# Kernel tuning notes

Measured on AMD Instinct MI355X. Metric: run time of the kernel, lower is better.

## Reference

```python
import jax, jax.numpy as jnp
import numpy as np

KERNEL_SIZE = 13
SIGMA_MIN, SIGMA_MAX = 0.4, 10.0
BETA, THRESHOLD = 0.95, 1.0


@jax.custom_vjp
def spike(x):
    # Heaviside forward, snntorch ATan surrogate backward (alpha=2)
    return (x > 0).astype(x.dtype)

def _spike_fwd(x):
    return spike(x), x

def _spike_bwd(x, g):
    return (g / (1.0 + (jnp.pi * x) ** 2),)

spike.defvjp(_spike_fwd, _spike_bwd)


def setup_inputs() -> dict:
    key = jax.random.key(0)
    k1, k2 = jax.random.split(key)
    B, C, T = 32, 224, 2048
    inp = jax.random.normal(k1, (B, 1, C, T), dtype=jnp.float32)
    linear_w = jax.random.normal(k2, (1, C), dtype=jnp.float32) * (1.0 / np.sqrt(C))
    return {"inp": inp, "linear_w": linear_w}


def _forward(inp, linear_w):
    x = inp[:, 0]  # [B, C, T]
    B, C, T = x.shape
    sigma_mean = 0.5 * (SIGMA_MIN + SIGMA_MAX)
    # adaptive sigma per (batch, time): Linear over channel axis, no bias
    w = sigma_mean + jnp.einsum('bct,c->bt', x, linear_w[0]) * (SIGMA_MAX - SIGMA_MIN)
    w = jnp.clip(w, SIGMA_MIN, SIGMA_MAX)  # [B, T]

    half = KERNEL_SIZE // 2
    r = jnp.linspace(-half, half, KERNEL_SIZE)
    r_all = jnp.linspace(-half * 10, half * 10, KERNEL_SIZE * 10)
    sig = w[..., None]  # [B, T, 1]
    kern = jnp.exp(-0.5 * (r / sig) ** 2)                       # [B, T, K]
    norm = jnp.exp(-0.5 * (r_all / sig) ** 2).sum(-1, keepdims=True)
    kern = kern / norm                                          # normalized over fine grid

    # adaptive gaussian smoothing along the CHANNEL axis (per timestep kernel)
    xt = jnp.transpose(x, (0, 2, 1))                            # [B, T, C]
    padded = jnp.pad(xt, ((0, 0), (0, 0), (half, half)))        # zero pad channels
    x_mean = sum(padded[:, :, k:k + C] * kern[:, :, k:k + 1]
                 for k in range(KERNEL_SIZE))                   # [B, T, C]
    x_mean = jnp.transpose(x_mean, (0, 2, 1))                   # [B, C, T]

    I = x - jax.nn.relu(x - x_mean)                             # soft min(x, x_mean)

    # Leaky-integrate-and-fire over time (snntorch Leaky, reset-by-subtract)
    def step(mem, I_t):
        reset = jax.lax.stop_gradient((mem > THRESHOLD).astype(I_t.dtype))
        mem = BETA * mem + I_t - reset * THRESHOLD
        spk = spike(mem - THRESHOLD)
        return mem, spk

    I_seq = jnp.transpose(I, (2, 0, 1))                         # [T, B, C]
    _, spk = jax.lax.scan(step, jnp.zeros((B, C), I.dtype), I_seq)
    spk = jnp.transpose(spk, (1, 2, 0))                         # [B, C, T]
    return spk[:, None]                                         # [B, 1, C, T]


def reference(inp, linear_w):
    return _forward(inp, linear_w)
```

## Files before the change

kernel.cpp:

```cpp
#include <hip/hip_runtime.h>
#include <math.h>

#define BB 32
#define CCH 224
#define TTT 2048
#define TPB 128
#define NT  (TTT/TPB)
#define CG  28
#define NCG (CCH/CG)
#define IROW 29
#define CPW 4
#define NSLOT 7

__device__ __forceinline__ void bar_lds() {
    asm volatile("s_waitcnt lgkmcnt(0)" ::: "memory");
    __builtin_amdgcn_s_barrier();
    asm volatile("" ::: "memory");
}

__global__ __launch_bounds__(1024) void kw(
    const float* __restrict__ x, const float* __restrict__ lw,
    double* __restrict__ kernG)
{
    __shared__ double sp[4][256];
    const int b  = blockIdx.y;
    const int tl = threadIdx.x & 255;
    const int q  = threadIdx.x >> 8;
    const int t  = blockIdx.x * 256 + tl;

    const float* xb  = x + (((size_t)(b * CCH + 56 * q)) << 11) + t;
    const float* lwq = lw + 56 * q;

    double p = 0.0;
    #pragma unroll 8
    for (int i = 0; i < 56; ++i)
        p += (double)xb[(size_t)i << 11] * (double)lwq[i];
    sp[q][tl] = p;
    __syncthreads();

    if (threadIdx.x < 256) {
        const int tt = blockIdx.x * 256 + threadIdx.x;
        double acc = (sp[0][threadIdx.x] + sp[1][threadIdx.x])
                   + (sp[2][threadIdx.x] + sp[3][threadIdx.x]);

        double w = 5.2 + acc * 9.6;
        w = fmin(fmax(w, 0.4), 10.0);
        double iw2 = 1.0 / (w * w);

        const double s = 120.0 / 129.0;
        double G  = exp(-0.125 * s * s * iw2);
        double G2 = G * G, G4 = G2 * G2, G8 = G4 * G4;
        double term = G, cmul = G8, norm = G;
        for (int u = 1; u <= 64; ++u) { term *= cmul; cmul *= G8; norm += term; }
        norm *= 2.0;

        double P = exp(-0.5 * iw2), P2 = P * P;
        double a = 1.0, bm = P, inv = 1.0 / norm;
        double* kr = kernG + (size_t)(b * TTT + tt) * 7;
        kr[0] = inv;
        #pragma unroll
        for (int d = 1; d <= 6; ++d) {
            a *= bm; bm *= P2;
            kr[d] = a * inv;
        }
    }
}

__global__ __launch_bounds__(512) void kf(
    const float* __restrict__ x, const double* __restrict__ kernG,
    float* __restrict__ out)
{
    __shared__ float IsR[NSLOT][TPB][IROW];
    __shared__ unsigned long long bitsb[2][2][CG][2];

    const int b   = blockIdx.y;
    const int cgi = blockIdx.x;
    const int c0  = cgi * CG;
    const int tid = threadIdx.x;
    const int ctid = tid - 64;

    const float*  xbase = x + (((size_t)(b * CCH)) << 11);
    const double* kbase = kernG + (size_t)(b * TTT) * 7;
    float* obase = out + (((size_t)(b * CCH + c0)) << 11);

    double mem = 0.0;
    bool   r   = false;

    const int tl = ctid & 63;
    const int cw = ctid >> 6;
    const int cb = CPW * cw;

    auto issue = [&](int tile, float (&rv)[2][16], double (&kv)[2][7]) {
        const int gt0 = tile * TPB;
        #pragma unroll
        for (int h = 0; h < 2; ++h) {
            const int tt = gt0 + tl + 64 * h;
            #pragma unroll
            for (int i = 0; i < 16; ++i) {
                int cr = c0 + cb - 6 + i;
                rv[h][i] = (cr >= 0 && cr < CCH)
                         ? xbase[((size_t)cr << 11) + tt] : 0.f;
            }
            const double* kp = kbase + (size_t)tt * 7;
            #pragma unroll
            for (int i = 0; i < 7; ++i) kv[h][i] = kp[i];
        }
    };

    auto conv_store = [&](int slot, float (&rv)[2][16], double (&kv)[2][7]) {
        #pragma unroll
        for (int h = 0; h < 2; ++h) {
            double kk7[7];
            #pragma unroll
            for (int i = 0; i < 7; ++i) kk7[i] = kv[h][i];
            double xv[16];
            #pragma unroll
            for (int i = 0; i < 16; ++i) xv[i] = (double)rv[h][i];
            #pragma unroll
            for (int c = 0; c < CPW; ++c) {
                double acc = 0.0;
                #pragma unroll
                for (int kk = 0; kk < 13; ++kk) {
                    int d = kk < 6 ? 6 - kk : kk - 6;
                    acc = fma(xv[c + kk], kk7[d], acc);
                }
                double xvv = xv[c + 6];
                double dd  = xvv - acc;
                IsR[slot][tl + 64 * h][cb + c] =
                    (float)(xvv - (dd > 0.0 ? dd : 0.0));
            }
        }
    };

    auto writeTile = [&](int t, int par, int seg) {
        const int t0o = t * TPB;
        const int c = ctid >> 4, q = ctid & 15;
        #pragma unroll
        for (int h = 0; h < 2; ++h) {
            unsigned long long bits = bitsb[par][seg][c][h] >> (4 * q);
            float4 v;
            v.x = (bits & 1ull) ? 1.0f : 0.0f;
            v.y = (bits & 2ull) ? 1.0f : 0.0f;
            v.z = (bits & 4ull) ? 1.0f : 0.0f;
            v.w = (bits & 8ull) ? 1.0f : 0.0f;
            *(float4*)(obase + ((size_t)c << 11) + t0o + 64 * h + 4 * q) = v;
        }
    };

    auto phase = [&](int k, float (&rv)[2][16], double (&kv)[2][7]) {
        if (tid >= 64) {
            if (k >= 2 && k <= 11) writeTile(k - 2, (k - 1) & 1, 0);
            if (k >= 7)            writeTile(k + 3, (k - 1) & 1, 1);
            if (k <= 10) conv_store((k + 5) % NSLOT, rv, kv);
            if (k <= 8)  issue(k + 7, rv, kv);
        } else {
            const int seg = tid >> 5;
            const int c   = tid & 31;
            const int myt = seg ? (k + 4) : (k - 1);
            const bool act = (c < CG) && (seg ? (k <= 11) : (k <= 10));
            __builtin_amdgcn_s_setprio(1);
            if (act) {
                const float* isb = &IsR[myt % NSLOT][0][c];
                unsigned long long bits0 = 0ull, bits1 = 0ull;
                double va[8], vb8[8], ca[8], cb2[8];
                #pragma unroll
                for (int j2 = 0; j2 < 8; ++j2) va[j2] = (double)isb[j2 * IROW];
                #pragma unroll
                for (int j2 = 0; j2 < 8; ++j2) ca[j2] = va[j2] - 1.0;
                for (int g2 = 0; g2 < TPB; g2 += 16) {
                    #pragma unroll
                    for (int j2 = 0; j2 < 8; ++j2)
                        vb8[j2] = (double)isb[(g2 + 8 + j2) * IROW];
                    #pragma unroll
                    for (int j2 = 0; j2 < 8; ++j2) cb2[j2] = vb8[j2] - 1.0;
                    #pragma unroll
                    for (int j2 = 0; j2 < 8; ++j2) {
                        double m1 = fma(0.95, mem, va[j2]);
                        double m2 = fma(0.95, mem, ca[j2]);
                        mem = r ? m2 : m1;
                        r = mem > 1.0;
                        const int s = g2 + j2;
                        unsigned long long bbit =
                            (unsigned long long)(r ? 1 : 0) << (s & 63);
                        if (s < 64) bits0 |= bbit; else bits1 |= bbit;
                    }
                    if (g2 + 16 < TPB) {
                        #pragma unroll
                        for (int j2 = 0; j2 < 8; ++j2)
                            va[j2] = (double)isb[(g2 + 16 + j2) * IROW];
                        #pragma unroll
                        for (int j2 = 0; j2 < 8; ++j2) ca[j2] = va[j2] - 1.0;
                    }
                    #pragma unroll
                    for (int j2 = 0; j2 < 8; ++j2) {
                        double m1 = fma(0.95, mem, vb8[j2]);
                        double m2 = fma(0.95, mem, cb2[j2]);
                        mem = r ? m2 : m1;
                        r = mem > 1.0;
                        const int s = g2 + 8 + j2;
                        unsigned long long bbit =
                            (unsigned long long)(r ? 1 : 0) << (s & 63);
                        if (s < 64) bits0 |= bbit; else bits1 |= bbit;
                    }
                }
                bitsb[k & 1][seg][c][0] = bits0;
                bitsb[k & 1][seg][c][1] = bits1;
            }
            __builtin_amdgcn_s_setprio(0);
        }
        bar_lds();
    };

    float  rA[2][16], rB[2][16];
    double kA[2][7],  kB[2][7];

    if (tid >= 64) {
        for (int i = 0; i < 6; ++i) {
            issue(i, rA, kA);
            conv_store(i, rA, kA);
        }
        issue(6, rB, kB);
        issue(7, rA, kA);
    }
    bar_lds();

    for (int kk = 1; kk <= 12; kk += 2) {
        phase(kk,     rB, kB);
        phase(kk + 1, rA, kA);
    }
}

extern "C" void kernel_launch(void* const* d_in, const int* in_sizes, int n_in,
                              void* d_out, int out_size, void* d_ws, size_t ws_size,
                              hipStream_t stream)
{
    const float* x  = (const float*)d_in[0];
    const float* lw = (const float*)d_in[1];
    float* out = (float*)d_out;

    double* kernG = (double*)d_ws;

    kw<<<dim3(TTT / 256, BB), 1024, 0, stream>>>(x, lw, kernG);
    kf<<<dim3(NCG, BB), 512, 0, stream>>>(x, kernG, out);
}
```

Before: 171.7 us.

## Transpose LDS current buffer, deepen slot ring, and restructure prologue pipeline

The staged current buffer is now laid out channel-major with padded rows, so the scan threads read consecutive timesteps with float2 LDS loads instead of strided scalar loads. The ring grows to eight slots using power-of-two indexing. The prologue software-pipelines global loads against convolution, and the main loop runs one fewer phase because the second scan segment starts one tile later. This aims to shorten the serial scan's LDS latency and the prologue stall, at the cost of more LDS and a retuned schedule that could be wrong.

```diff
diff --git a/kernel.cpp b/kernel.cpp
--- a/kernel.cpp
+++ b/kernel.cpp
@@ -8,9 +8,9 @@
 #define NT  (TTT/TPB)
 #define CG  28
 #define NCG (CCH/CG)
-#define IROW 29
 #define CPW 4
-#define NSLOT 7
+#define NSLOT 8
+#define TROW 130
 
 __device__ __forceinline__ void bar_lds() {
     asm volatile("s_waitcnt lgkmcnt(0)" ::: "memory");
@@ -70,7 +70,7 @@
     const float* __restrict__ x, const double* __restrict__ kernG,
     float* __restrict__ out)
 {
-    __shared__ float IsR[NSLOT][TPB][IROW];
+    __shared__ float IsT[NSLOT][CG][TROW];
     __shared__ unsigned long long bitsb[2][2][CG][2];
 
     const int b   = blockIdx.y;
@@ -126,7 +126,7 @@
                 }
                 double xvv = xv[c + 6];
                 double dd  = xvv - acc;
-                IsR[slot][tl + 64 * h][cb + c] =
+                IsT[slot][cb + c][tl + 64 * h] =
                     (float)(xvv - (dd > 0.0 ? dd : 0.0));
             }
         }
@@ -149,28 +149,34 @@
 
     auto phase = [&](int k, float (&rv)[2][16], double (&kv)[2][7]) {
         if (tid >= 64) {
-            if (k >= 2 && k <= 11) writeTile(k - 2, (k - 1) & 1, 0);
-            if (k >= 7)            writeTile(k + 3, (k - 1) & 1, 1);
-            if (k <= 10) conv_store((k + 5) % NSLOT, rv, kv);
-            if (k <= 8)  issue(k + 7, rv, kv);
-        } else {
+            if (k >= 2)  writeTile(k - 2, (k - 1) & 1, 0);
+            if (k >= 6)  writeTile(k + 4, (k - 1) & 1, 1);
+            if (k <= 9)  conv_store((k + 6) & 7, rv, kv);
+            if (k <= 7)  issue(k + 8, rv, kv);
+        } else if (k <= 10) {
             const int seg = tid >> 5;
             const int c   = tid & 31;
-            const int myt = seg ? (k + 4) : (k - 1);
-            const bool act = (c < CG) && (seg ? (k <= 11) : (k <= 10));
+            const int myt = seg ? (k + 5) : (k - 1);
             __builtin_amdgcn_s_setprio(1);
-            if (act) {
-                const float* isb = &IsR[myt % NSLOT][0][c];
+            if (c < CG) {
+                const float* isb = &IsT[myt & 7][c][0];
                 unsigned long long bits0 = 0ull, bits1 = 0ull;
                 double va[8], vb8[8], ca[8], cb2[8];
                 #pragma unroll
-                for (int j2 = 0; j2 < 8; ++j2) va[j2] = (double)isb[j2 * IROW];
+                for (int j2 = 0; j2 < 4; ++j2) {
+                    float2 p2 = *(const float2*)(isb + 2 * j2);
+                    va[2 * j2]     = (double)p2.x;
+                    va[2 * j2 + 1] = (double)p2.y;
+                }
                 #pragma unroll
                 for (int j2 = 0; j2 < 8; ++j2) ca[j2] = va[j2] - 1.0;
                 for (int g2 = 0; g2 < TPB; g2 += 16) {
                     #pragma unroll
-                    for (int j2 = 0; j2 < 8; ++j2)
-                        vb8[j2] = (double)isb[(g2 + 8 + j2) * IROW];
+                    for (int j2 = 0; j2 < 4; ++j2) {
+                        float2 p2 = *(const float2*)(isb + g2 + 8 + 2 * j2);
+                        vb8[2 * j2]     = (double)p2.x;
+                        vb8[2 * j2 + 1] = (double)p2.y;
+                    }
                     #pragma unroll
                     for (int j2 = 0; j2 < 8; ++j2) cb2[j2] = vb8[j2] - 1.0;
                     #pragma unroll
@@ -186,8 +192,11 @@
                     }
                     if (g2 + 16 < TPB) {
                         #pragma unroll
-                        for (int j2 = 0; j2 < 8; ++j2)
-                            va[j2] = (double)isb[(g2 + 16 + j2) * IROW];
+                        for (int j2 = 0; j2 < 4; ++j2) {
+                            float2 p2 = *(const float2*)(isb + g2 + 16 + 2 * j2);
+                            va[2 * j2]     = (double)p2.x;
+                            va[2 * j2 + 1] = (double)p2.y;
+                        }
                         #pragma unroll
                         for (int j2 = 0; j2 < 8; ++j2) ca[j2] = va[j2] - 1.0;
                     }
@@ -215,18 +224,20 @@
     double kA[2][7],  kB[2][7];
 
     if (tid >= 64) {
-        for (int i = 0; i < 6; ++i) {
-            issue(i, rA, kA);
-            conv_store(i, rA, kA);
-        }
-        issue(6, rB, kB);
-        issue(7, rA, kA);
+        issue(0, rA, kA); issue(1, rB, kB);
+        conv_store(0, rA, kA); issue(2, rA, kA);
+        conv_store(1, rB, kB); issue(3, rB, kB);
+        conv_store(2, rA, kA); issue(4, rA, kA);
+        conv_store(3, rB, kB); issue(5, rB, kB);
+        conv_store(4, rA, kA); issue(6, rA, kA);
+        conv_store(5, rB, kB); issue(7, rB, kB);
+        conv_store(6, rA, kA); issue(8, rA, kA);
     }
     bar_lds();
 
-    for (int kk = 1; kk <= 12; kk += 2) {
-        phase(kk,     rB, kB);
-        phase(kk + 1, rA, kA);
+    for (int kk = 1; kk <= 11; kk += 2) {
+        phase(kk, rB, kB);
+        if (kk + 1 <= 11) phase(kk + 1, rA, kA);
     }
 }
 
```

After: 219.2 us. +27.7%, slower.
